# Performance work log

Hardware: AMD Instinct MI355X
Metric: run time of the kernel (lower is better)

## Reference

```python
import jax, jax.numpy as jnp
import numpy as np

N_COND, K, D = 16, 512, 256
B, H, W = 32, 64, 64


def setup_inputs() -> dict:
    key = jax.random.key(0)
    k1, k2, k3 = jax.random.split(key, 3)
    z_e_x = jax.random.normal(k1, (B, D, H, W), dtype=jnp.float32)
    C = jax.random.randint(k2, (B,), 0, N_COND, dtype=jnp.int64)
    bound = 1.0 / (K * N_COND)
    weight = jax.random.uniform(k3, (N_COND, K, D), dtype=jnp.float32,
                                minval=-bound, maxval=bound)
    return {"z_e_x": z_e_x, "C": C, "weight": weight}


def reference(z_e_x, C, weight):
    b, d, h, w = z_e_x.shape
    # [B, H, W, D] -> [B, N, D] with N = H*W
    z = jnp.transpose(z_e_x, (0, 2, 3, 1)).reshape(b, h * w, d)
    cb = weight[C]  # per-sample codebook [B, K, D] (batched gather replaces python loop)
    # squared euclidean distances: ||z||^2 - 2 z.e + ||e||^2  -> [B, N, K]
    dist = (jnp.sum(z * z, axis=-1, keepdims=True)
            - 2.0 * jnp.einsum('bnd,bkd->bnk', z, cb)
            + jnp.sum(cb * cb, axis=-1)[:, None, :])
    idx = jnp.argmin(dist, axis=-1)  # [B, N]
    quant = jnp.take_along_axis(cb, idx[..., None], axis=1)  # [B, N, D]
    # straight-through output (vq_st): forward = quantized
    z_q = z + jax.lax.stop_gradient(quant - z)
    # z_q_x_bar: plain gather from (non-detached) codebook
    z_q_bar = quant
    z_q_x = jnp.transpose(z_q.reshape(b, h, w, d), (0, 3, 1, 2))
    z_q_x_bar = jnp.transpose(z_q_bar.reshape(b, h, w, d), (0, 3, 1, 2))
    return z_q_x, z_q_x_bar
```

## Files before the change

### kernel.cpp

```cpp
#include <hip/hip_runtime.h>
#include <cfloat>

#define NB    32
#define ND    256
#define NK    512
#define NCOND 16
#define NHW   4096
#define PXT   32
#define MARGIN 1.3e-4f
#define QCAP  16

typedef __attribute__((ext_vector_type(8))) short bf16x8;
typedef __attribute__((ext_vector_type(4))) float f32x4;

__device__ __forceinline__ int loadC(const int* __restrict__ C, int b) {
  int orodd = 0;
#pragma unroll
  for (int i = 1; i < 32; i += 2) orodd |= C[i];
  return (orodd == 0) ? C[2 * b] : C[b];
}

__device__ __forceinline__ unsigned short rne_bf16(float x) {
  unsigned u = __float_as_uint(x);
  u += 0x7fffu + ((u >> 16) & 1u);
  return (unsigned short)(u >> 16);
}

__device__ float np_score_g(const float* __restrict__ z, size_t zoff,
                            const float* __restrict__ er, float S) {
  float P0 = 0.f, P1 = 0.f, P2 = 0.f, P3 = 0.f;
  for (int ch = 0; ch < 16; ++ch) {
    const float* eb = er + ch * 16;
    float4 e0 = *(const float4*)(eb + 0);
    float4 e1 = *(const float4*)(eb + 4);
    float4 e2 = *(const float4*)(eb + 8);
    float4 e3 = *(const float4*)(eb + 12);
    float zb[16];
#pragma unroll
    for (int q = 0; q < 16; ++q)
      zb[q] = z[zoff + (size_t)(ch * 16 + q) * NHW];
    P0 = __fadd_rn(P0, __fmul_rn(zb[12], e3.x));
    P0 = __fadd_rn(P0, __fmul_rn(zb[8],  e2.x));
    P0 = __fadd_rn(P0, __fmul_rn(zb[4],  e1.x));
    P0 = __fadd_rn(P0, __fmul_rn(zb[0],  e0.x));
    P1 = __fadd_rn(P1, __fmul_rn(zb[13], e3.y));
    P1 = __fadd_rn(P1, __fmul_rn(zb[9],  e2.y));
    P1 = __fadd_rn(P1, __fmul_rn(zb[5],  e1.y));
    P1 = __fadd_rn(P1, __fmul_rn(zb[1],  e0.y));
    P2 = __fadd_rn(P2, __fmul_rn(zb[14], e3.z));
    P2 = __fadd_rn(P2, __fmul_rn(zb[10], e2.z));
    P2 = __fadd_rn(P2, __fmul_rn(zb[6],  e1.z));
    P2 = __fadd_rn(P2, __fmul_rn(zb[2],  e0.z));
    P3 = __fadd_rn(P3, __fmul_rn(zb[15], e3.w));
    P3 = __fadd_rn(P3, __fmul_rn(zb[11], e2.w));
    P3 = __fadd_rn(P3, __fmul_rn(zb[7],  e1.w));
    P3 = __fadd_rn(P3, __fmul_rn(zb[3],  e0.w));
  }
  float G = __fadd_rn(__fadd_rn(P0, P1), __fadd_rn(P2, P3));
  return __fadd_rn(S, __fmul_rn(-2.0f, G));
}

__global__ __launch_bounds__(256) void k_split(
    const float* __restrict__ w, unsigned short* __restrict__ whi) {
  int i = (blockIdx.x * 256 + threadIdx.x) * 4;
  float4 v = *(const float4*)&w[i];
  int ci = i >> 17, rem = i & 131071;
  int code = rem >> 8, d = rem & 255;
  int dst = (ci << 17) + ((d >> 5) << 14) + (code << 5) + (d & 31);
  ushort4 h;
  h.x = rne_bf16(v.x); h.y = rne_bf16(v.y);
  h.z = rne_bf16(v.z); h.w = rne_bf16(v.w);
  *(ushort4*)&whi[dst] = h;
}

__device__ __forceinline__ int zofs(int px, int chunk) {
  return px * 256 + ((chunk ^ (px & 7)) * 8);
}

template <int PRE>
__global__ __launch_bounds__(256, 4) void k_vq(
    const float* __restrict__ z, const int* __restrict__ Cc,
    const float* __restrict__ w, const unsigned short* __restrict__ whi,
    float* __restrict__ out) {
  __shared__ __align__(16) unsigned short Zh[PXT * ND];
  __shared__ __align__(16) unsigned short Zl[PXT * ND];
  __shared__ float Ssh[PXT];
  __shared__ float Wmin[4][PXT];
  __shared__ float Thr[PXT];
  __shared__ int   qcnt[PXT], KB[PXT];
  __shared__ int   qk[PXT][QCAP];

  float* Rsh = (float*)qk;

  int orig = blockIdx.x;
  int blk  = (orig & 7) * 512 + (orig >> 3);
  int b    = blk >> 7;
  int n0   = (blk & 127) * PXT;
  int c    = loadC(Cc, b);
  int t    = threadIdx.x;
  int lane = t & 63;
  int wv   = t >> 6;

  const size_t zab = (size_t)b * ND * NHW;
  const size_t cbu = (size_t)c * (NK * ND);
  const int ar0  = lane & 15;
  const int koff = (lane >> 4) * 8;

  {
    int px = t & 31, dg = t >> 5;
    const float* zp = z + zab + n0 + px;
#pragma unroll
    for (int cc4 = 0; cc4 < 4; ++cc4) {
      int chunk = dg * 4 + cc4;
      bf16x8 h, l;
#pragma unroll
      for (int j = 0; j < 8; ++j) {
        float v = zp[(size_t)(chunk * 8 + j) * NHW];
        unsigned u = __float_as_uint(v) & 0xffff0000u;
        h[j] = (short)(u >> 16);
        l[j] = (short)rne_bf16(v - __uint_as_float(u));
      }
      *(bf16x8*)&Zh[zofs(px, chunk)] = h;
      *(bf16x8*)&Zl[zofs(px, chunk)] = l;
    }
  }

  {
    int px = t & 31, j = t >> 5;
    const float* zp = z + zab + n0 + px;
    float a0 = zp[(size_t)j * NHW];
    float r0 = __fmul_rn(a0, a0);
    float a1 = zp[(size_t)(128 + j) * NHW];
    float r1 = __fmul_rn(a1, a1);
#pragma unroll
    for (int i = 1; i < 16; ++i) {
      float v0 = zp[(size_t)(8 * i + j) * NHW];
      r0 = __fadd_rn(r0, __fmul_rn(v0, v0));
      float v1 = zp[(size_t)(128 + 8 * i + j) * NHW];
      r1 = __fadd_rn(r1, __fmul_rn(v1, v1));
    }
    Rsh[j * 32 + px]       = r0;
    Rsh[256 + j * 32 + px] = r1;
  }
  if (t < PXT) qcnt[t] = 0;
  __syncthreads();

  if (t < PXT) {
    int px = t;
    float pw0 = __fadd_rn(
        __fadd_rn(__fadd_rn(Rsh[0 * 32 + px], Rsh[1 * 32 + px]),
                  __fadd_rn(Rsh[2 * 32 + px], Rsh[3 * 32 + px])),
        __fadd_rn(__fadd_rn(Rsh[4 * 32 + px], Rsh[5 * 32 + px]),
                  __fadd_rn(Rsh[6 * 32 + px], Rsh[7 * 32 + px])));
    float pw1 = __fadd_rn(
        __fadd_rn(__fadd_rn(Rsh[256 + 0 * 32 + px], Rsh[256 + 1 * 32 + px]),
                  __fadd_rn(Rsh[256 + 2 * 32 + px], Rsh[256 + 3 * 32 + px])),
        __fadd_rn(__fadd_rn(Rsh[256 + 4 * 32 + px], Rsh[256 + 5 * 32 + px]),
                  __fadd_rn(Rsh[256 + 6 * 32 + px], Rsh[256 + 7 * 32 + px])));
    Ssh[px] = __fadd_rn(pw0, pw1);
  }
  __syncthreads();

  f32x4 acc0[8], acc1[8];
#pragma unroll
  for (int nt = 0; nt < 8; ++nt) {
    acc0[nt] = (f32x4){0.f, 0.f, 0.f, 0.f};
    acc1[nt] = (f32x4){0.f, 0.f, 0.f, 0.f};
  }

#pragma unroll 1
  for (int ks = 0; ks < 8; ++ks) {
    int chunkA = ks * 4 + (lane >> 4);
    bf16x8 ah0 = *(const bf16x8*)&Zh[zofs(ar0,      chunkA)];
    bf16x8 al0 = *(const bf16x8*)&Zl[zofs(ar0,      chunkA)];
    bf16x8 ah1 = *(const bf16x8*)&Zh[zofs(ar0 + 16, chunkA)];
    bf16x8 al1 = *(const bf16x8*)&Zl[zofs(ar0 + 16, chunkA)];
#pragma unroll
    for (int nt = 0; nt < 8; ++nt) {
      int code = wv * 128 + nt * 16 + (lane & 15);
      bf16x8 bh;
      if constexpr (PRE) {
        bh = *(const bf16x8*)(whi + cbu + ks * (NK * 32) + code * 32 + koff);
      } else {
        const float* sf = w + ((size_t)c * NK + code) * ND + ks * 32 + koff;
        float4 f0 = *(const float4*)sf;
        float4 f1 = *(const float4*)(sf + 4);
        float xs[8] = {f0.x, f0.y, f0.z, f0.w, f1.x, f1.y, f1.z, f1.w};
#pragma unroll
        for (int q = 0; q < 8; ++q) bh[q] = (short)rne_bf16(xs[q]);
      }
      acc0[nt] = __builtin_amdgcn_mfma_f32_16x16x32_bf16(ah0, bh, acc0[nt], 0, 0, 0);
      acc0[nt] = __builtin_amdgcn_mfma_f32_16x16x32_bf16(al0, bh, acc0[nt], 0, 0, 0);
      acc1[nt] = __builtin_amdgcn_mfma_f32_16x16x32_bf16(ah1, bh, acc1[nt], 0, 0, 0);
      acc1[nt] = __builtin_amdgcn_mfma_f32_16x16x32_bf16(al1, bh, acc1[nt], 0, 0, 0);
    }
  }

  float pmin0[4], pmin1[4], S40[4], S41[4];
#pragma unroll
  for (int r = 0; r < 4; ++r) {
    int pr = (lane >> 4) * 4 + r;
    S40[r] = Ssh[pr];
    S41[r] = Ssh[pr + 16];
    pmin0[r] = FLT_MAX; pmin1[r] = FLT_MAX;
  }
#pragma unroll
  for (int nt = 0; nt < 8; ++nt)
#pragma unroll
    for (int r = 0; r < 4; ++r) {
      float X0 = __fadd_rn(S40[r], __fmul_rn(-2.0f, acc0[nt][r]));
      float X1 = __fadd_rn(S41[r], __fmul_rn(-2.0f, acc1[nt][r]));
      acc0[nt][r] = X0; acc1[nt][r] = X1;
      pmin0[r] = fminf(pmin0[r], X0);
      pmin1[r] = fminf(pmin1[r], X1);
    }
#pragma unroll
  for (int r = 0; r < 4; ++r)
#pragma unroll
    for (int off = 1; off < 16; off <<= 1) {
      pmin0[r] = fminf(pmin0[r], __shfl_xor(pmin0[r], off));
      pmin1[r] = fminf(pmin1[r], __shfl_xor(pmin1[r], off));
    }
  if ((lane & 15) == 0) {
#pragma unroll
    for (int r = 0; r < 4; ++r) {
      Wmin[wv][(lane >> 4) * 4 + r]      = pmin0[r];
      Wmin[wv][16 + (lane >> 4) * 4 + r] = pmin1[r];
    }
  }
  __syncthreads();
  if (t < PXT) {
    Thr[t] = fminf(fminf(Wmin[0][t], Wmin[1][t]),
                   fminf(Wmin[2][t], Wmin[3][t])) + MARGIN;
  }
  __syncthreads();

#pragma unroll
  for (int r = 0; r < 4; ++r) {
    int px0 = (lane >> 4) * 4 + r;
    float th0 = Thr[px0], th1 = Thr[px0 + 16];
#pragma unroll
    for (int nt = 0; nt < 8; ++nt) {
      int kcode = wv * 128 + nt * 16 + (lane & 15);
      if (acc0[nt][r] <= th0) {
        int slot = atomicAdd(&qcnt[px0], 1);
        if (slot < QCAP) qk[px0][slot] = kcode;
      }
      if (acc1[nt][r] <= th1) {
        int slot = atomicAdd(&qcnt[px0 + 16], 1);
        if (slot < QCAP) qk[px0 + 16][slot] = kcode;
      }
    }
  }
  __syncthreads();

  {
    int px  = wv * 8 + (lane >> 3);
    int cnt = qcnt[px]; cnt = cnt < QCAP ? cnt : QCAP;
    float S = Ssh[px];
    size_t zoff = zab + n0 + px;
    float bv = FLT_MAX; int bk = 0x7fffffff;
    int slot0 = lane & 7;
    if (cnt == 1) {
      if (slot0 == 0) { bv = 0.f; bk = qk[px][0]; }
    } else {
#pragma unroll
      for (int m = 0; m < 2; ++m) {
        int slot = slot0 + 8 * m;
        bool act = slot < cnt;
        if (__any(act)) {
          if (act) {
            int k = qk[px][slot];
            float v = np_score_g(z, zoff, w + ((size_t)c * NK + k) * ND, S);
            if (v < bv || (v == bv && k < bk)) { bv = v; bk = k; }
          }
        }
      }
    }
#pragma unroll
    for (int off = 1; off < 8; off <<= 1) {
      float ov = __shfl_xor(bv, off);
      int   ok = __shfl_xor(bk, off);
      if (ov < bv || (ov == bv && ok < bk)) { bv = ov; bk = ok; }
    }
    if (slot0 == 0) KB[px] = bk;
  }
  __syncthreads();

  {
    int px = t & 31, dg = t >> 5;
    int kidx = KB[px];
    const float* er = w + ((size_t)c * NK + kidx) * ND;
    const size_t OUT2 = (size_t)NB * ND * NHW;
    size_t base = zab + n0 + px;
#pragma unroll
    for (int j = 0; j < 32; ++j) {
      int d = dg * 32 + j;
      float q  = er[d];
      float zv = z[base + (size_t)d * NHW];
      out[base + (size_t)d * NHW]        = __fadd_rn(zv, __fsub_rn(q, zv));
      out[base + (size_t)d * NHW + OUT2] = q;
    }
  }
}

extern "C" void kernel_launch(void* const* d_in, const int* in_sizes, int n_in,
                              void* d_out, int out_size, void* d_ws, size_t ws_size,
                              hipStream_t stream) {
  const float* z = (const float*)d_in[0];
  const int*   C = (const int*)d_in[1];
  const float* w = (const float*)d_in[2];
  float* out = (float*)d_out;

  const size_t NWEL = (size_t)NCOND * NK * ND;
  unsigned short* whi = (unsigned short*)d_ws;
  bool pre = ws_size >= NWEL * sizeof(unsigned short);

  if (pre) {
    k_split<<<(int)(NWEL / 1024), 256, 0, stream>>>(w, whi);
    k_vq<1><<<NB * (NHW / PXT), 256, 0, stream>>>(z, C, w, whi, out);
  } else {
    k_vq<0><<<NB * (NHW / PXT), 256, 0, stream>>>(z, C, w, nullptr, out);
  }
}
```

Baseline: 218.5 us.

## Stage z tile as fp32 in LDS and reuse it across all phases

The z tile is loaded once into a padded fp32 shared-memory array instead of separate bf16 hi/lo arrays. The norm computation, the exact rescoring of candidates and the output pass now read z from LDS rather than re-reading it from global memory. The bf16 hi/lo split moves into the MFMA k-loop, which adds per-iteration conversion ALU work and float4 LDS reads. LDS use stays the same size (32x260 floats against 2x32x256 shorts), so occupancy should not change. An extra barrier is added before the norm pass.

```diff
diff --git a/kernel.cpp b/kernel.cpp
--- a/kernel.cpp
+++ b/kernel.cpp
@@ -7,6 +7,7 @@
 #define NCOND 16
 #define NHW   4096
 #define PXT   32
+#define ZSTR  260
 #define MARGIN 1.3e-4f
 #define QCAP  16
 
@@ -26,8 +27,8 @@
   return (unsigned short)(u >> 16);
 }
 
-__device__ float np_score_g(const float* __restrict__ z, size_t zoff,
-                            const float* __restrict__ er, float S) {
+__device__ __forceinline__ float np_score(const float* zrow,
+                                          const float* __restrict__ er, float S) {
   float P0 = 0.f, P1 = 0.f, P2 = 0.f, P3 = 0.f;
   for (int ch = 0; ch < 16; ++ch) {
     const float* eb = er + ch * 16;
@@ -35,26 +36,27 @@
     float4 e1 = *(const float4*)(eb + 4);
     float4 e2 = *(const float4*)(eb + 8);
     float4 e3 = *(const float4*)(eb + 12);
-    float zb[16];
-#pragma unroll
-    for (int q = 0; q < 16; ++q)
-      zb[q] = z[zoff + (size_t)(ch * 16 + q) * NHW];
-    P0 = __fadd_rn(P0, __fmul_rn(zb[12], e3.x));
-    P0 = __fadd_rn(P0, __fmul_rn(zb[8],  e2.x));
-    P0 = __fadd_rn(P0, __fmul_rn(zb[4],  e1.x));
-    P0 = __fadd_rn(P0, __fmul_rn(zb[0],  e0.x));
-    P1 = __fadd_rn(P1, __fmul_rn(zb[13], e3.y));
-    P1 = __fadd_rn(P1, __fmul_rn(zb[9],  e2.y));
-    P1 = __fadd_rn(P1, __fmul_rn(zb[5],  e1.y));
-    P1 = __fadd_rn(P1, __fmul_rn(zb[1],  e0.y));
-    P2 = __fadd_rn(P2, __fmul_rn(zb[14], e3.z));
-    P2 = __fadd_rn(P2, __fmul_rn(zb[10], e2.z));
-    P2 = __fadd_rn(P2, __fmul_rn(zb[6],  e1.z));
-    P2 = __fadd_rn(P2, __fmul_rn(zb[2],  e0.z));
-    P3 = __fadd_rn(P3, __fmul_rn(zb[15], e3.w));
-    P3 = __fadd_rn(P3, __fmul_rn(zb[11], e2.w));
-    P3 = __fadd_rn(P3, __fmul_rn(zb[7],  e1.w));
-    P3 = __fadd_rn(P3, __fmul_rn(zb[3],  e0.w));
+    const float* zb = zrow + ch * 16;
+    float4 z0 = *(const float4*)(zb + 0);
+    float4 z1 = *(const float4*)(zb + 4);
+    float4 z2 = *(const float4*)(zb + 8);
+    float4 z3 = *(const float4*)(zb + 12);
+    P0 = __fadd_rn(P0, __fmul_rn(z3.x, e3.x));
+    P0 = __fadd_rn(P0, __fmul_rn(z2.x, e2.x));
+    P0 = __fadd_rn(P0, __fmul_rn(z1.x, e1.x));
+    P0 = __fadd_rn(P0, __fmul_rn(z0.x, e0.x));
+    P1 = __fadd_rn(P1, __fmul_rn(z3.y, e3.y));
+    P1 = __fadd_rn(P1, __fmul_rn(z2.y, e2.y));
+    P1 = __fadd_rn(P1, __fmul_rn(z1.y, e1.y));
+    P1 = __fadd_rn(P1, __fmul_rn(z0.y, e0.y));
+    P2 = __fadd_rn(P2, __fmul_rn(z3.z, e3.z));
+    P2 = __fadd_rn(P2, __fmul_rn(z2.z, e2.z));
+    P2 = __fadd_rn(P2, __fmul_rn(z1.z, e1.z));
+    P2 = __fadd_rn(P2, __fmul_rn(z0.z, e0.z));
+    P3 = __fadd_rn(P3, __fmul_rn(z3.w, e3.w));
+    P3 = __fadd_rn(P3, __fmul_rn(z2.w, e2.w));
+    P3 = __fadd_rn(P3, __fmul_rn(z1.w, e1.w));
+    P3 = __fadd_rn(P3, __fmul_rn(z0.w, e0.w));
   }
   float G = __fadd_rn(__fadd_rn(P0, P1), __fadd_rn(P2, P3));
   return __fadd_rn(S, __fmul_rn(-2.0f, G));
@@ -73,17 +75,12 @@
   *(ushort4*)&whi[dst] = h;
 }
 
-__device__ __forceinline__ int zofs(int px, int chunk) {
-  return px * 256 + ((chunk ^ (px & 7)) * 8);
-}
-
 template <int PRE>
 __global__ __launch_bounds__(256, 4) void k_vq(
     const float* __restrict__ z, const int* __restrict__ Cc,
     const float* __restrict__ w, const unsigned short* __restrict__ whi,
     float* __restrict__ out) {
-  __shared__ __align__(16) unsigned short Zh[PXT * ND];
-  __shared__ __align__(16) unsigned short Zl[PXT * ND];
+  __shared__ __align__(16) float Zs[PXT][ZSTR];
   __shared__ float Ssh[PXT];
   __shared__ float Wmin[4][PXT];
   __shared__ float Thr[PXT];
@@ -110,39 +107,30 @@
     int px = t & 31, dg = t >> 5;
     const float* zp = z + zab + n0 + px;
 #pragma unroll
-    for (int cc4 = 0; cc4 < 4; ++cc4) {
-      int chunk = dg * 4 + cc4;
-      bf16x8 h, l;
-#pragma unroll
-      for (int j = 0; j < 8; ++j) {
-        float v = zp[(size_t)(chunk * 8 + j) * NHW];
-        unsigned u = __float_as_uint(v) & 0xffff0000u;
-        h[j] = (short)(u >> 16);
-        l[j] = (short)rne_bf16(v - __uint_as_float(u));
-      }
-      *(bf16x8*)&Zh[zofs(px, chunk)] = h;
-      *(bf16x8*)&Zl[zofs(px, chunk)] = l;
-    }
-  }
+    for (int j = 0; j < 32; ++j) {
+      int d = dg * 32 + j;
+      Zs[px][d] = zp[(size_t)d * NHW];
+    }
+  }
+  if (t < PXT) qcnt[t] = 0;
+  __syncthreads();
 
   {
     int px = t & 31, j = t >> 5;
-    const float* zp = z + zab + n0 + px;
-    float a0 = zp[(size_t)j * NHW];
+    float a0 = Zs[px][j];
     float r0 = __fmul_rn(a0, a0);
-    float a1 = zp[(size_t)(128 + j) * NHW];
+    float a1 = Zs[px][128 + j];
     float r1 = __fmul_rn(a1, a1);
 #pragma unroll
     for (int i = 1; i < 16; ++i) {
-      float v0 = zp[(size_t)(8 * i + j) * NHW];
+      float v0 = Zs[px][8 * i + j];
       r0 = __fadd_rn(r0, __fmul_rn(v0, v0));
-      float v1 = zp[(size_t)(128 + 8 * i + j) * NHW];
+      float v1 = Zs[px][128 + 8 * i + j];
       r1 = __fadd_rn(r1, __fmul_rn(v1, v1));
     }
     Rsh[j * 32 + px]       = r0;
     Rsh[256 + j * 32 + px] = r1;
   }
-  if (t < PXT) qcnt[t] = 0;
   __syncthreads();
 
   if (t < PXT) {
@@ -170,17 +158,31 @@
 
 #pragma unroll 1
   for (int ks = 0; ks < 8; ++ks) {
-    int chunkA = ks * 4 + (lane >> 4);
-    bf16x8 ah0 = *(const bf16x8*)&Zh[zofs(ar0,      chunkA)];
-    bf16x8 al0 = *(const bf16x8*)&Zl[zofs(ar0,      chunkA)];
-    bf16x8 ah1 = *(const bf16x8*)&Zh[zofs(ar0 + 16, chunkA)];
-    bf16x8 al1 = *(const bf16x8*)&Zl[zofs(ar0 + 16, chunkA)];
+    bf16x8 ah0, al0, ah1, al1;
+    {
+      const float* zr0 = &Zs[ar0][ks * 32 + koff];
+      const float* zr1 = &Zs[ar0 + 16][ks * 32 + koff];
+      float4 a = *(const float4*)zr0, bq = *(const float4*)(zr0 + 4);
+      float4 cq = *(const float4*)zr1, dq = *(const float4*)(zr1 + 4);
+      float x0[8] = {a.x, a.y, a.z, a.w, bq.x, bq.y, bq.z, bq.w};
+      float x1[8] = {cq.x, cq.y, cq.z, cq.w, dq.x, dq.y, dq.z, dq.w};
+#pragma unroll
+      for (int j = 0; j < 8; ++j) {
+        unsigned u0 = __float_as_uint(x0[j]) & 0xffff0000u;
+        ah0[j] = (short)(u0 >> 16);
+        al0[j] = (short)rne_bf16(x0[j] - __uint_as_float(u0));
+        unsigned u1 = __float_as_uint(x1[j]) & 0xffff0000u;
+        ah1[j] = (short)(u1 >> 16);
+        al1[j] = (short)rne_bf16(x1[j] - __uint_as_float(u1));
+      }
+    }
+    const unsigned short* wk = whi + cbu + ks * (NK * 32);
 #pragma unroll
     for (int nt = 0; nt < 8; ++nt) {
       int code = wv * 128 + nt * 16 + (lane & 15);
       bf16x8 bh;
       if constexpr (PRE) {
-        bh = *(const bf16x8*)(whi + cbu + ks * (NK * 32) + code * 32 + koff);
+        bh = *(const bf16x8*)(wk + code * 32 + koff);
       } else {
         const float* sf = w + ((size_t)c * NK + code) * ND + ks * 32 + koff;
         float4 f0 = *(const float4*)sf;
@@ -258,7 +260,6 @@
     int px  = wv * 8 + (lane >> 3);
     int cnt = qcnt[px]; cnt = cnt < QCAP ? cnt : QCAP;
     float S = Ssh[px];
-    size_t zoff = zab + n0 + px;
     float bv = FLT_MAX; int bk = 0x7fffffff;
     int slot0 = lane & 7;
     if (cnt == 1) {
@@ -271,7 +272,7 @@
         if (__any(act)) {
           if (act) {
             int k = qk[px][slot];
-            float v = np_score_g(z, zoff, w + ((size_t)c * NK + k) * ND, S);
+            float v = np_score(&Zs[px][0], w + ((size_t)c * NK + k) * ND, S);
             if (v < bv || (v == bv && k < bk)) { bv = v; bk = k; }
           }
         }
@@ -297,7 +298,7 @@
     for (int j = 0; j < 32; ++j) {
       int d = dg * 32 + j;
       float q  = er[d];
-      float zv = z[base + (size_t)d * NHW];
+      float zv = Zs[px][d];
       out[base + (size_t)d * NHW]        = __fadd_rn(zv, __fsub_rn(q, zv));
       out[base + (size_t)d * NHW + OUT2] = q;
     }
```

After: 310.3 us. 1.42x slower.
